# Performance work log

Measured on AMD Instinct MI355X. Metric: run time of the kernel, lower is better.

The kernel has to match this reference:

```python
import jax, jax.numpy as jnp
import numpy as np

EPS = 1e-5
SLOPE = 0.01  # LeakyReLU default negative_slope


def _bn4d(y, g, b):
    # training-mode BatchNorm4d: stats over batch + all 4 spatial dims, biased var
    ax = (0, 2, 3, 4, 5)
    mu = y.mean(axis=ax, keepdims=True)
    var = ((y - mu) ** 2).mean(axis=ax, keepdims=True)
    sh = (1, -1, 1, 1, 1, 1)
    return (y - mu) / jnp.sqrt(var + EPS) * g.reshape(sh) + b.reshape(sh)


def _lrelu(y):
    return jnp.where(y >= 0, y, SLOPE * y)


def setup_inputs() -> dict:
    key = jax.random.key(0)
    ks = jax.random.split(key, 4)
    x = jax.random.uniform(ks[0], (2, 1, 48, 48, 48, 48), dtype=jnp.float32)
    w1 = jax.random.normal(ks[1], (3, 1), dtype=jnp.float32) * 0.5
    w2 = jax.random.normal(ks[2], (6, 3, 2, 2, 2, 2), dtype=jnp.float32) * 0.15
    wt = jax.random.normal(ks[3], (6, 3, 2, 2, 2, 2), dtype=jnp.float32) * 0.15
    return {
        "x": x,
        "w1": w1, "g1": jnp.ones(3, jnp.float32), "b1": jnp.zeros(3, jnp.float32),
        "w2": w2, "g2": jnp.ones(6, jnp.float32), "b2": jnp.zeros(6, jnp.float32),
        "wt": wt, "g3": jnp.ones(3, jnp.float32), "b3": jnp.zeros(3, jnp.float32),
    }


def reference(x, w1, g1, b1, w2, g2, b2, wt, g3, b3):
    # Conv4d(1->3, k=1, s=1, bias=False): pointwise channel mix
    y = jnp.einsum('oc,bcijkl->boijkl', w1, x)
    y = _lrelu(_bn4d(y, g1, b1))

    # Conv4d(3->6, k=2, s=2, bias=False): non-overlapping 2^4 block contraction
    B, C, D1, D2, D3, D4 = y.shape
    yb = y.reshape(B, C, D1 // 2, 2, D2 // 2, 2, D3 // 2, 2, D4 // 2, 2)
    y = jnp.einsum('bcipjqkrls,ocpqrs->boijkl', yb, w2)
    y = _lrelu(_bn4d(y, g2, b2))

    # ConvTranspose4d(6->3, k=2, s=2, bias=False): exact inverse block expansion
    # torch transpose-conv weight layout: (in_ch=6, out_ch=3, 2,2,2,2)
    z = jnp.einsum('bcijkl,copqrs->boipjqkrls', y, wt)
    B, O = z.shape[0], z.shape[1]
    d1, d2, d3, d4 = z.shape[2], z.shape[4], z.shape[6], z.shape[8]
    y = z.reshape(B, O, 2 * d1, 2 * d2, 2 * d3, 2 * d4)
    y = _bn4d(y, g3, b3)
    return jax.nn.sigmoid(y)
```

## Files before the change

kernel.cpp:

```cpp
#include <hip/hip_runtime.h>

#define BATCH 2
#define P1 5308416
#define NX 10616832
#define P2 331776
#define NPOS 663552
#define N2CH 663552.0
#define NZCH 10616832.0
#define EPS 1e-5
#define SLOPE 0.01f
#define NBANK 16

typedef float f32x2 __attribute__((ext_vector_type(2)));


__device__ __forceinline__ float lrelu(float v) { return v >= 0.f ? v : SLOPE * v; }

__device__ __forceinline__ double wred(double v) {
#pragma unroll
    for (int off = 32; off > 0; off >>= 1) v += __shfl_down(v, off, 64);
    return v;
}

__global__ __launch_bounds__(256) void k1_stats_x(const float4* __restrict__ x4,
                                                  double* __restrict__ dx) {
    int gid = blockIdx.x * 256 + threadIdx.x;
    double s = 0.0, q = 0.0;
#pragma unroll 1
    for (int i = gid; i < NX / 4; i += 1296 * 256) {
        float4 v = x4[i];
        s += (double)v.x + (double)v.y + (double)v.z + (double)v.w;
        q += (double)v.x * v.x + (double)v.y * v.y + (double)v.z * v.z + (double)v.w * v.w;
    }
    s = wred(s); q = wred(q);
    __shared__ double lds[4][2];
    int lane = threadIdx.x & 63, wv = threadIdx.x >> 6;
    if (lane == 0) { lds[wv][0] = s; lds[wv][1] = q; }
    __syncthreads();
    if (threadIdx.x < 2) {
        double t = lds[0][threadIdx.x] + lds[1][threadIdx.x] + lds[2][threadIdx.x] + lds[3][threadIdx.x];
        atomicAdd(&dx[(blockIdx.x & (NBANK - 1)) * 2 + threadIdx.x], t);
    }
}

__global__ __launch_bounds__(256) void k2_conv(const float* __restrict__ x,
                                               const float* __restrict__ w1,
                                               const float* __restrict__ g1,
                                               const float* __restrict__ b1,
                                               const float* __restrict__ w2,
                                               const double* __restrict__ dx,
                                               float* __restrict__ y2,
                                               double* __restrict__ d2) {
    double sx = 0.0, qx = 0.0;
#pragma unroll
    for (int bk = 0; bk < NBANK; ++bk) { sx += dx[bk * 2]; qx += dx[bk * 2 + 1]; }
    double mux = sx / (double)NX;
    double vax = qx / (double)NX - mux * mux;
    float a1[3], c1[3];
#pragma unroll
    for (int c = 0; c < 3; ++c) {
        double w = (double)w1[c];
        double inv = 1.0 / sqrt(w * w * vax + EPS);
        double a = w * (double)g1[c] * inv;
        a1[c] = (float)a;
        c1[c] = (float)((double)b1[c] - mux * a);
    }

    double dsum[6] = {0, 0, 0, 0, 0, 0}, dsq[6] = {0, 0, 0, 0, 0, 0};
#pragma unroll 1
    for (int it = 0; it < 4; ++it) {
        int t = blockIdx.x * 256 + threadIdx.x + it * 165888;
        int b = t / P2, rem = t % P2;
        int l0 = rem % 24, t1 = rem / 24;
        int k0 = t1 % 24, t2 = t1 / 24;
        int j0 = t2 % 24, i0 = t2 / 24;
        const float* xb = x + (size_t)b * P1 + (size_t)i0 * 221184 + j0 * 4608 + k0 * 96 + l0 * 2;
        float acc[6] = {0, 0, 0, 0, 0, 0};
#pragma unroll
        for (int p = 0; p < 2; ++p)
#pragma unroll
            for (int q = 0; q < 2; ++q)
#pragma unroll
                for (int r = 0; r < 2; ++r) {
                    const f32x2 xv = *(const f32x2*)(xb + p * 110592 + q * 2304 + r * 48);
#pragma unroll
                    for (int s = 0; s < 2; ++s) {
                        float xs = xv[s];
                        int m = p * 8 + q * 4 + r * 2 + s;
#pragma unroll
                        for (int c = 0; c < 3; ++c) {
                            float tt = lrelu(a1[c] * xs + c1[c]);
#pragma unroll
                            for (int o = 0; o < 6; ++o) acc[o] += w2[o * 48 + c * 16 + m] * tt;
                        }
                    }
                }
#pragma unroll
        for (int o = 0; o < 6; ++o) {
            y2[(size_t)(b * 6 + o) * P2 + rem] = acc[o];
            dsum[o] += (double)acc[o];
            dsq[o] += (double)acc[o] * acc[o];
        }
    }
    __shared__ double lds[4][12];
    int lane = threadIdx.x & 63, wv = threadIdx.x >> 6;
#pragma unroll
    for (int o = 0; o < 6; ++o) {
        double v = wred(dsum[o]); if (lane == 0) lds[wv][o] = v;
        v = wred(dsq[o]);         if (lane == 0) lds[wv][6 + o] = v;
    }
    __syncthreads();
    if (threadIdx.x < 12) {
        double t = lds[0][threadIdx.x] + lds[1][threadIdx.x] + lds[2][threadIdx.x] + lds[3][threadIdx.x];
        atomicAdd(&d2[(blockIdx.x & (NBANK - 1)) * 12 + threadIdx.x], t);
    }
}

__global__ __launch_bounds__(256) void k3_gram(const float* __restrict__ y2,
                                               const float* __restrict__ g2,
                                               const float* __restrict__ b2,
                                               const double* __restrict__ d2,
                                               double* __restrict__ d3) {
    float a2[6], c2[6];
#pragma unroll
    for (int c = 0; c < 6; ++c) {
        double s = 0.0, q = 0.0;
#pragma unroll
        for (int bk = 0; bk < NBANK; ++bk) { s += d2[bk * 12 + c]; q += d2[bk * 12 + 6 + c]; }
        double mu = s / N2CH;
        double va = q / N2CH - mu * mu;
        double a = (double)g2[c] / sqrt(va + EPS);
        a2[c] = (float)a;
        c2[c] = (float)((double)b2[c] - mu * a);
    }
    double S[6] = {0, 0, 0, 0, 0, 0};
    double G[21] = {0};
#pragma unroll 1
    for (int it = 0; it < 4; ++it) {
        int t = blockIdx.x * 256 + threadIdx.x + it * 165888;
        int b = t / P2, rem = t % P2;
        float yn[6];
#pragma unroll
        for (int c = 0; c < 6; ++c) {
            float v = y2[(size_t)(b * 6 + c) * P2 + rem];
            yn[c] = lrelu(a2[c] * v + c2[c]);
            S[c] += (double)yn[c];
        }
        int gi = 0;
#pragma unroll
        for (int c = 0; c < 6; ++c)
#pragma unroll
            for (int cc = c; cc < 6; ++cc) { G[gi] += (double)yn[c] * yn[cc]; ++gi; }
    }
    __shared__ double lds[4][27];
    int lane = threadIdx.x & 63, wv = threadIdx.x >> 6;
#pragma unroll
    for (int i = 0; i < 6; ++i) { double v = wred(S[i]); if (lane == 0) lds[wv][i] = v; }
#pragma unroll
    for (int i = 0; i < 21; ++i) { double v = wred(G[i]); if (lane == 0) lds[wv][6 + i] = v; }
    __syncthreads();
    if (threadIdx.x < 27) {
        double t = lds[0][threadIdx.x] + lds[1][threadIdx.x] + lds[2][threadIdx.x] + lds[3][threadIdx.x];
        atomicAdd(&d3[(blockIdx.x & (NBANK - 1)) * 27 + threadIdx.x], t);
    }
}

__global__ void k4_params(const double* __restrict__ d2, const double* __restrict__ d3,
                          const float* __restrict__ wt,
                          const float* __restrict__ g2v, const float* __restrict__ b2v,
                          const float* __restrict__ g3, const float* __restrict__ b3,
                          float* __restrict__ params) {
    __shared__ double S[6], G[21], s2[12];
    int t = threadIdx.x;
    if (t < 27) {
        double a = 0.0;
        for (int bk = 0; bk < NBANK; ++bk) a += d3[bk * 27 + t];
        if (t < 6) S[t] = a; else G[t - 6] = a;
    }
    if (t >= 32 && t < 44) {
        double a = 0.0;
        for (int bk = 0; bk < NBANK; ++bk) a += d2[bk * 12 + (t - 32)];
        s2[t - 32] = a;
    }
    __syncthreads();
    if (t < 6) {
        int c = t;
        double mu = s2[c] / N2CH;
        double va = s2[6 + c] / N2CH - mu * mu;
        double a = (double)g2v[c] / sqrt(va + EPS);
        params[c] = (float)a;
        params[6 + c] = (float)((double)b2v[c] - mu * a);
    }
    if (t < 3) {
        int o = t;
        double sumz = 0.0, ssq = 0.0;
        for (int c = 0; c < 6; ++c) {
            double wsum = 0.0;
            for (int m = 0; m < 16; ++m) wsum += (double)wt[c * 48 + o * 16 + m];
            sumz += S[c] * wsum;
        }
        for (int c = 0; c < 6; ++c)
            for (int cc = 0; cc < 6; ++cc) {
                double ww = 0.0;
                for (int m = 0; m < 16; ++m) ww += (double)wt[c * 48 + o * 16 + m] * wt[cc * 48 + o * 16 + m];
                int aa = c < cc ? c : cc, bb = c < cc ? cc : c;
                int gidx = aa * 6 - aa * (aa + 1) / 2 + bb;
                ssq += G[gidx] * ww;
            }
        double mu = sumz / NZCH;
        double va = ssq / NZCH - mu * mu;
        double a = (double)g3[o] / sqrt(va + EPS);
        params[12 + o] = (float)a;
        params[15 + o] = (float)((double)b3[o] - mu * a);
    }
}

__global__ __launch_bounds__(256) void k5_expand(const float* __restrict__ y2,
                                                 const float* __restrict__ wt,
                                                 const float* __restrict__ params,
                                                 float* __restrict__ out) {
    int t = blockIdx.x * 256 + threadIdx.x;
    int b = t / P2, rem = t % P2;
    int l0 = rem % 24, t1 = rem / 24;
    int k0 = t1 % 24, t2 = t1 / 24;
    int j0 = t2 % 24, i0 = t2 / 24;
    float yn[6];
#pragma unroll
    for (int c = 0; c < 6; ++c) {
        float v = y2[(size_t)(b * 6 + c) * P2 + rem];
        yn[c] = lrelu(params[c] * v + params[6 + c]);
    }
    size_t obase = (size_t)b * 15925248 + (size_t)i0 * 221184 + j0 * 4608 + k0 * 96 + l0 * 2;
#pragma unroll
    for (int o = 0; o < 3; ++o) {
        float a3 = params[12 + o], c3 = params[15 + o];
#pragma unroll
        for (int p = 0; p < 2; ++p)
#pragma unroll
            for (int q = 0; q < 2; ++q)
#pragma unroll
                for (int r = 0; r < 2; ++r) {
                    f32x2 res;
#pragma unroll
                    for (int s = 0; s < 2; ++s) {
                        int m = p * 8 + q * 4 + r * 2 + s;
                        float z = 0.f;
#pragma unroll
                        for (int c = 0; c < 6; ++c) z += yn[c] * wt[c * 48 + o * 16 + m];
                        float v = a3 * z + c3;
                        res[s] = 1.f / (1.f + __expf(-v));
                    }
                    __builtin_nontemporal_store(res, (f32x2*)(out + obase + (size_t)o * P1 + p * 110592 + q * 2304 + r * 48));
                }
    }
}

extern "C" void kernel_launch(void* const* d_in, const int* in_sizes, int n_in,
                              void* d_out, int out_size, void* d_ws, size_t ws_size,
                              hipStream_t stream) {
    const float* x  = (const float*)d_in[0];
    const float* w1 = (const float*)d_in[1];
    const float* g1 = (const float*)d_in[2];
    const float* b1 = (const float*)d_in[3];
    const float* w2 = (const float*)d_in[4];
    const float* g2 = (const float*)d_in[5];
    const float* b2 = (const float*)d_in[6];
    const float* wt = (const float*)d_in[7];
    const float* g3 = (const float*)d_in[8];
    const float* b3 = (const float*)d_in[9];
    float* out = (float*)d_out;

    char* ws = (char*)d_ws;
    double* dx     = (double*)(ws);
    double* d2     = (double*)(ws + 256);
    double* d3     = (double*)(ws + 1792);
    float*  params = (float*)(ws + 5248);
    float*  y2     = (float*)(ws + 8192);

    (void)hipMemsetAsync(d_ws, 0, 5248, stream);
    k1_stats_x<<<1296, 256, 0, stream>>>((const float4*)x, dx);
    k2_conv<<<648, 256, 0, stream>>>(x, w1, g1, b1, w2, dx, y2, d2);
    k3_gram<<<648, 256, 0, stream>>>(y2, g2, b2, d2, d3);
    k4_params<<<1, 64, 0, stream>>>(d2, d3, wt, g2, b2, g3, b3, params);
    k5_expand<<<2592, 256, 0, stream>>>(y2, wt, params, out);
}
```

Baseline: 362.7 us.

## Vectorize loads/stores, switch per-thread stats to fp32, remap expand threads for contiguous writes

Several kernels are reworked at once. k1 uses a fixed 8-load unrolled loop with fp32 accumulation. k2 has each thread handle two adjacent positions with 16-byte x loads and transposed w2 in LDS, and k3 likewise handles two positions per thread, both with fp32 partial sums. k5 is remapped so each thread writes one 16-byte contiguous output chunk per channel with per-thread weights. The aim is fewer, wider memory transactions and cheaper reductions than double-precision math, at the risk of reduced accuracy in the fp32 partial sums.

```diff
diff --git a/kernel.cpp b/kernel.cpp
--- a/kernel.cpp
+++ b/kernel.cpp
@@ -1,10 +1,8 @@
 #include <hip/hip_runtime.h>
 
-#define BATCH 2
 #define P1 5308416
 #define NX 10616832
 #define P2 331776
-#define NPOS 663552
 #define N2CH 663552.0
 #define NZCH 10616832.0
 #define EPS 1e-5
@@ -12,156 +10,184 @@
 #define NBANK 16
 
 typedef float f32x2 __attribute__((ext_vector_type(2)));
+typedef float f32x4 __attribute__((ext_vector_type(4)));
 
 
 __device__ __forceinline__ float lrelu(float v) { return v >= 0.f ? v : SLOPE * v; }
 
-__device__ __forceinline__ double wred(double v) {
+__device__ __forceinline__ float wredf(float v) {
 #pragma unroll
     for (int off = 32; off > 0; off >>= 1) v += __shfl_down(v, off, 64);
     return v;
 }
 
-__global__ __launch_bounds__(256) void k1_stats_x(const float4* __restrict__ x4,
+__global__ __launch_bounds__(256) void k1_stats_x(const f32x4* __restrict__ x4,
                                                   double* __restrict__ dx) {
     int gid = blockIdx.x * 256 + threadIdx.x;
-    double s = 0.0, q = 0.0;
-#pragma unroll 1
-    for (int i = gid; i < NX / 4; i += 1296 * 256) {
-        float4 v = x4[i];
-        s += (double)v.x + (double)v.y + (double)v.z + (double)v.w;
-        q += (double)v.x * v.x + (double)v.y * v.y + (double)v.z * v.z + (double)v.w * v.w;
-    }
-    s = wred(s); q = wred(q);
-    __shared__ double lds[4][2];
+    float s = 0.f, q = 0.f;
+#pragma unroll
+    for (int k = 0; k < 8; ++k) {
+        f32x4 v = x4[gid + k * 331776];
+        s += v.x + v.y + v.z + v.w;
+        q += v.x * v.x + v.y * v.y + v.z * v.z + v.w * v.w;
+    }
+    s = wredf(s); q = wredf(q);
+    __shared__ float lds[4][2];
     int lane = threadIdx.x & 63, wv = threadIdx.x >> 6;
     if (lane == 0) { lds[wv][0] = s; lds[wv][1] = q; }
     __syncthreads();
     if (threadIdx.x < 2) {
-        double t = lds[0][threadIdx.x] + lds[1][threadIdx.x] + lds[2][threadIdx.x] + lds[3][threadIdx.x];
+        double t = (double)lds[0][threadIdx.x] + lds[1][threadIdx.x] + lds[2][threadIdx.x] + lds[3][threadIdx.x];
         atomicAdd(&dx[(blockIdx.x & (NBANK - 1)) * 2 + threadIdx.x], t);
     }
 }
 
-__global__ __launch_bounds__(256) void k2_conv(const float* __restrict__ x,
-                                               const float* __restrict__ w1,
-                                               const float* __restrict__ g1,
-                                               const float* __restrict__ b1,
-                                               const float* __restrict__ w2,
-                                               const double* __restrict__ dx,
-                                               float* __restrict__ y2,
-                                               double* __restrict__ d2) {
-    double sx = 0.0, qx = 0.0;
-#pragma unroll
-    for (int bk = 0; bk < NBANK; ++bk) { sx += dx[bk * 2]; qx += dx[bk * 2 + 1]; }
-    double mux = sx / (double)NX;
-    double vax = qx / (double)NX - mux * mux;
+__global__ __launch_bounds__(256, 4) void k2_conv(const float* __restrict__ x,
+                                                  const float* __restrict__ w1,
+                                                  const float* __restrict__ g1,
+                                                  const float* __restrict__ b1,
+                                                  const float* __restrict__ w2,
+                                                  const double* __restrict__ dx,
+                                                  float* __restrict__ y2,
+                                                  double* __restrict__ d2) {
+    __shared__ __align__(16) float w2s[48 * 8];
+    __shared__ float p1s[6];
+    for (int idx = threadIdx.x; idx < 288; idx += 256) {
+        int o = idx / 48, cm = idx % 48;
+        w2s[cm * 8 + o] = w2[idx];
+    }
+    if (threadIdx.x < 3) {
+        double sx = 0.0, qx = 0.0;
+#pragma unroll
+        for (int bk = 0; bk < NBANK; ++bk) { sx += dx[bk * 2]; qx += dx[bk * 2 + 1]; }
+        double mux = sx / (double)NX;
+        double vax = qx / (double)NX - mux * mux;
+        int c = threadIdx.x;
+        double w = (double)w1[c];
+        double a = w * (double)g1[c] / sqrt(w * w * vax + EPS);
+        p1s[c] = (float)a;
+        p1s[3 + c] = (float)((double)b1[c] - mux * a);
+    }
+    __syncthreads();
     float a1[3], c1[3];
 #pragma unroll
-    for (int c = 0; c < 3; ++c) {
-        double w = (double)w1[c];
-        double inv = 1.0 / sqrt(w * w * vax + EPS);
-        double a = w * (double)g1[c] * inv;
-        a1[c] = (float)a;
-        c1[c] = (float)((double)b1[c] - mux * a);
-    }
-
-    double dsum[6] = {0, 0, 0, 0, 0, 0}, dsq[6] = {0, 0, 0, 0, 0, 0};
-#pragma unroll 1
-    for (int it = 0; it < 4; ++it) {
-        int t = blockIdx.x * 256 + threadIdx.x + it * 165888;
-        int b = t / P2, rem = t % P2;
-        int l0 = rem % 24, t1 = rem / 24;
-        int k0 = t1 % 24, t2 = t1 / 24;
-        int j0 = t2 % 24, i0 = t2 / 24;
-        const float* xb = x + (size_t)b * P1 + (size_t)i0 * 221184 + j0 * 4608 + k0 * 96 + l0 * 2;
-        float acc[6] = {0, 0, 0, 0, 0, 0};
-#pragma unroll
-        for (int p = 0; p < 2; ++p)
-#pragma unroll
-            for (int q = 0; q < 2; ++q)
-#pragma unroll
-                for (int r = 0; r < 2; ++r) {
-                    const f32x2 xv = *(const f32x2*)(xb + p * 110592 + q * 2304 + r * 48);
-#pragma unroll
-                    for (int s = 0; s < 2; ++s) {
-                        float xs = xv[s];
-                        int m = p * 8 + q * 4 + r * 2 + s;
-#pragma unroll
-                        for (int c = 0; c < 3; ++c) {
-                            float tt = lrelu(a1[c] * xs + c1[c]);
-#pragma unroll
-                            for (int o = 0; o < 6; ++o) acc[o] += w2[o * 48 + c * 16 + m] * tt;
-                        }
-                    }
-                }
-#pragma unroll
-        for (int o = 0; o < 6; ++o) {
-            y2[(size_t)(b * 6 + o) * P2 + rem] = acc[o];
-            dsum[o] += (double)acc[o];
-            dsq[o] += (double)acc[o] * acc[o];
+    for (int c = 0; c < 3; ++c) { a1[c] = p1s[c]; c1[c] = p1s[3 + c]; }
+
+    int t = blockIdx.x * 256 + threadIdx.x;
+    int pos0 = t * 2;
+    int b = pos0 / P2, rem = pos0 % P2;
+    int l0 = rem % 24, t1 = rem / 24;
+    int k0 = t1 % 24, t2 = t1 / 24;
+    int j0 = t2 % 24, i0 = t2 / 24;
+    const float* xb = x + (size_t)b * P1 + (size_t)i0 * 221184 + j0 * 4608 + k0 * 96 + l0 * 2;
+
+    f32x4 xq[8];
+#pragma unroll
+    for (int p = 0; p < 2; ++p)
+#pragma unroll
+        for (int q = 0; q < 2; ++q)
+#pragma unroll
+            for (int r = 0; r < 2; ++r)
+                xq[p * 4 + q * 2 + r] = *(const f32x4*)(xb + p * 110592 + q * 2304 + r * 48);
+
+    float acc0[6] = {0, 0, 0, 0, 0, 0}, acc1[6] = {0, 0, 0, 0, 0, 0};
+#pragma unroll
+    for (int pqr = 0; pqr < 8; ++pqr) {
+#pragma unroll
+        for (int s = 0; s < 2; ++s) {
+            int m = pqr * 2 + s;
+            float xs0 = xq[pqr][s];
+            float xs1 = xq[pqr][2 + s];
+#pragma unroll
+            for (int c = 0; c < 3; ++c) {
+                float tt0 = lrelu(a1[c] * xs0 + c1[c]);
+                float tt1 = lrelu(a1[c] * xs1 + c1[c]);
+                int base = (c * 16 + m) * 8;
+                f32x4 w4 = *(const f32x4*)&w2s[base];
+                f32x2 w2v = *(const f32x2*)&w2s[base + 4];
+                acc0[0] += w4.x * tt0; acc1[0] += w4.x * tt1;
+                acc0[1] += w4.y * tt0; acc1[1] += w4.y * tt1;
+                acc0[2] += w4.z * tt0; acc1[2] += w4.z * tt1;
+                acc0[3] += w4.w * tt0; acc1[3] += w4.w * tt1;
+                acc0[4] += w2v.x * tt0; acc1[4] += w2v.x * tt1;
+                acc0[5] += w2v.y * tt0; acc1[5] += w2v.y * tt1;
+            }
         }
     }
-    __shared__ double lds[4][12];
+    float sum[6], sq[6];
+#pragma unroll
+    for (int o = 0; o < 6; ++o) {
+        f32x2 st; st.x = acc0[o]; st.y = acc1[o];
+        *(f32x2*)(y2 + (size_t)(b * 6 + o) * P2 + rem) = st;
+        sum[o] = acc0[o] + acc1[o];
+        sq[o] = acc0[o] * acc0[o] + acc1[o] * acc1[o];
+    }
+    __shared__ float lds[4][12];
     int lane = threadIdx.x & 63, wv = threadIdx.x >> 6;
 #pragma unroll
     for (int o = 0; o < 6; ++o) {
-        double v = wred(dsum[o]); if (lane == 0) lds[wv][o] = v;
-        v = wred(dsq[o]);         if (lane == 0) lds[wv][6 + o] = v;
+        float v = wredf(sum[o]); if (lane == 0) lds[wv][o] = v;
+        v = wredf(sq[o]);        if (lane == 0) lds[wv][6 + o] = v;
     }
     __syncthreads();
     if (threadIdx.x < 12) {
-        double t = lds[0][threadIdx.x] + lds[1][threadIdx.x] + lds[2][threadIdx.x] + lds[3][threadIdx.x];
-        atomicAdd(&d2[(blockIdx.x & (NBANK - 1)) * 12 + threadIdx.x], t);
-    }
-}
-
-__global__ __launch_bounds__(256) void k3_gram(const float* __restrict__ y2,
-                                               const float* __restrict__ g2,
-                                               const float* __restrict__ b2,
-                                               const double* __restrict__ d2,
-                                               double* __restrict__ d3) {
-    float a2[6], c2[6];
-#pragma unroll
-    for (int c = 0; c < 6; ++c) {
+        double t2d = (double)lds[0][threadIdx.x] + lds[1][threadIdx.x] + lds[2][threadIdx.x] + lds[3][threadIdx.x];
+        atomicAdd(&d2[(blockIdx.x & (NBANK - 1)) * 12 + threadIdx.x], t2d);
+    }
+}
+
+__global__ __launch_bounds__(256, 4) void k3_gram(const float* __restrict__ y2,
+                                                  const float* __restrict__ g2,
+                                                  const float* __restrict__ b2,
+                                                  const double* __restrict__ d2,
+                                                  double* __restrict__ d3) {
+    __shared__ float p2s[12];
+    if (threadIdx.x < 6) {
+        int c = threadIdx.x;
         double s = 0.0, q = 0.0;
 #pragma unroll
         for (int bk = 0; bk < NBANK; ++bk) { s += d2[bk * 12 + c]; q += d2[bk * 12 + 6 + c]; }
         double mu = s / N2CH;
         double va = q / N2CH - mu * mu;
         double a = (double)g2[c] / sqrt(va + EPS);
-        a2[c] = (float)a;
-        c2[c] = (float)((double)b2[c] - mu * a);
-    }
-    double S[6] = {0, 0, 0, 0, 0, 0};
-    double G[21] = {0};
-#pragma unroll 1
-    for (int it = 0; it < 4; ++it) {
-        int t = blockIdx.x * 256 + threadIdx.x + it * 165888;
-        int b = t / P2, rem = t % P2;
-        float yn[6];
-#pragma unroll
-        for (int c = 0; c < 6; ++c) {
-            float v = y2[(size_t)(b * 6 + c) * P2 + rem];
-            yn[c] = lrelu(a2[c] * v + c2[c]);
-            S[c] += (double)yn[c];
-        }
+        p2s[c] = (float)a;
+        p2s[6 + c] = (float)((double)b2[c] - mu * a);
+    }
+    __syncthreads();
+    float a2[6], c2[6];
+#pragma unroll
+    for (int c = 0; c < 6; ++c) { a2[c] = p2s[c]; c2[c] = p2s[6 + c]; }
+
+    int t = blockIdx.x * 256 + threadIdx.x;
+    int pos0 = t * 2;
+    int b = pos0 / P2, rem = pos0 % P2;
+    float yn0[6], yn1[6];
+#pragma unroll
+    for (int c = 0; c < 6; ++c) {
+        f32x2 v = *(const f32x2*)(y2 + (size_t)(b * 6 + c) * P2 + rem);
+        yn0[c] = lrelu(a2[c] * v.x + c2[c]);
+        yn1[c] = lrelu(a2[c] * v.y + c2[c]);
+    }
+    float S[6], G[21];
+#pragma unroll
+    for (int c = 0; c < 6; ++c) S[c] = yn0[c] + yn1[c];
+    {
         int gi = 0;
 #pragma unroll
         for (int c = 0; c < 6; ++c)
 #pragma unroll
-            for (int cc = c; cc < 6; ++cc) { G[gi] += (double)yn[c] * yn[cc]; ++gi; }
-    }
-    __shared__ double lds[4][27];
+            for (int cc = c; cc < 6; ++cc) { G[gi] = yn0[c] * yn0[cc] + yn1[c] * yn1[cc]; ++gi; }
+    }
+    __shared__ float lds[4][27];
     int lane = threadIdx.x & 63, wv = threadIdx.x >> 6;
 #pragma unroll
-    for (int i = 0; i < 6; ++i) { double v = wred(S[i]); if (lane == 0) lds[wv][i] = v; }
-#pragma unroll
-    for (int i = 0; i < 21; ++i) { double v = wred(G[i]); if (lane == 0) lds[wv][6 + i] = v; }
+    for (int i = 0; i < 6; ++i) { float v = wredf(S[i]); if (lane == 0) lds[wv][i] = v; }
+#pragma unroll
+    for (int i = 0; i < 21; ++i) { float v = wredf(G[i]); if (lane == 0) lds[wv][6 + i] = v; }
     __syncthreads();
     if (threadIdx.x < 27) {
-        double t = lds[0][threadIdx.x] + lds[1][threadIdx.x] + lds[2][threadIdx.x] + lds[3][threadIdx.x];
-        atomicAdd(&d3[(blockIdx.x & (NBANK - 1)) * 27 + threadIdx.x], t);
+        double td = (double)lds[0][threadIdx.x] + lds[1][threadIdx.x] + lds[2][threadIdx.x] + lds[3][threadIdx.x];
+        atomicAdd(&d3[(blockIdx.x & (NBANK - 1)) * 27 + threadIdx.x], td);
     }
 }
 
@@ -220,38 +246,58 @@
                                                  const float* __restrict__ params,
                                                  float* __restrict__ out) {
     int t = blockIdx.x * 256 + threadIdx.x;
-    int b = t / P2, rem = t % P2;
-    int l0 = rem % 24, t1 = rem / 24;
-    int k0 = t1 % 24, t2 = t1 / 24;
-    int j0 = t2 % 24, i0 = t2 / 24;
-    float yn[6];
+    int row = t / 12, d = t % 12;
+    int b = row / 110592, rr = row % 110592;
+    int i = rr / 2304, r2 = rr % 2304;
+    int j = r2 / 48, k = r2 % 48;
+    int i0 = i >> 1, p = i & 1;
+    int j0 = j >> 1, q = j & 1;
+    int k0 = k >> 1, r = k & 1;
+
+    float a2[6], c2[6], a3[3], c3[3];
+#pragma unroll
+    for (int c = 0; c < 6; ++c) { a2[c] = params[c]; c2[c] = params[6 + c]; }
+#pragma unroll
+    for (int o = 0; o < 3; ++o) { a3[o] = params[12 + o]; c3[o] = params[15 + o]; }
+
+    float W[3][2][6];
+    int wbase = p * 8 + q * 4 + r * 2;
+#pragma unroll
+    for (int o = 0; o < 3; ++o)
+#pragma unroll
+        for (int s = 0; s < 2; ++s)
+#pragma unroll
+            for (int c = 0; c < 6; ++c)
+                W[o][s][c] = wt[c * 48 + o * 16 + wbase + s];
+
+    const float* yb = y2 + (size_t)b * 6 * P2 + (size_t)i0 * 13824 + j0 * 576 + k0 * 24 + 2 * d;
+    float yn0[6], yn1[6];
 #pragma unroll
     for (int c = 0; c < 6; ++c) {
-        float v = y2[(size_t)(b * 6 + c) * P2 + rem];
-        yn[c] = lrelu(params[c] * v + params[6 + c]);
-    }
-    size_t obase = (size_t)b * 15925248 + (size_t)i0 * 221184 + j0 * 4608 + k0 * 96 + l0 * 2;
+        f32x2 v = *(const f32x2*)(yb + (size_t)c * P2);
+        yn0[c] = lrelu(a2[c] * v.x + c2[c]);
+        yn1[c] = lrelu(a2[c] * v.y + c2[c]);
+    }
+
+    size_t ob = (size_t)b * 15925248 + (size_t)i * 110592 + (size_t)j * 2304 + k * 48 + 4 * d;
 #pragma unroll
     for (int o = 0; o < 3; ++o) {
-        float a3 = params[12 + o], c3 = params[15 + o];
-#pragma unroll
-        for (int p = 0; p < 2; ++p)
-#pragma unroll
-            for (int q = 0; q < 2; ++q)
-#pragma unroll
-                for (int r = 0; r < 2; ++r) {
-                    f32x2 res;
-#pragma unroll
-                    for (int s = 0; s < 2; ++s) {
-                        int m = p * 8 + q * 4 + r * 2 + s;
-                        float z = 0.f;
-#pragma unroll
-                        for (int c = 0; c < 6; ++c) z += yn[c] * wt[c * 48 + o * 16 + m];
-                        float v = a3 * z + c3;
-                        res[s] = 1.f / (1.f + __expf(-v));
-                    }
-                    __builtin_nontemporal_store(res, (f32x2*)(out + obase + (size_t)o * P1 + p * 110592 + q * 2304 + r * 48));
-                }
+        f32x4 res;
+#pragma unroll
+        for (int dd = 0; dd < 4; ++dd) {
+            int s = dd & 1;
+            float z = 0.f;
+            if (dd < 2) {
+#pragma unroll
+                for (int c = 0; c < 6; ++c) z += yn0[c] * W[o][s][c];
+            } else {
+#pragma unroll
+                for (int c = 0; c < 6; ++c) z += yn1[c] * W[o][s][c];
+            }
+            float v = a3[o] * z + c3[o];
+            res[dd] = 1.f / (1.f + __expf(-v));
+        }
+        __builtin_nontemporal_store(res, (f32x4*)(out + ob + (size_t)o * P1));
     }
 }
 
@@ -278,9 +324,9 @@
     float*  y2     = (float*)(ws + 8192);
 
     (void)hipMemsetAsync(d_ws, 0, 5248, stream);
-    k1_stats_x<<<1296, 256, 0, stream>>>((const float4*)x, dx);
-    k2_conv<<<648, 256, 0, stream>>>(x, w1, g1, b1, w2, dx, y2, d2);
-    k3_gram<<<648, 256, 0, stream>>>(y2, g2, b2, d2, d3);
+    k1_stats_x<<<1296, 256, 0, stream>>>((const f32x4*)x, dx);
+    k2_conv<<<1296, 256, 0, stream>>>(x, w1, g1, b1, w2, dx, y2, d2);
+    k3_gram<<<1296, 256, 0, stream>>>(y2, g2, b2, d2, d3);
     k4_params<<<1, 64, 0, stream>>>(d2, d3, wt, g2, b2, g3, b3, params);
-    k5_expand<<<2592, 256, 0, stream>>>(y2, wt, params, out);
-}
+    k5_expand<<<10368, 256, 0, stream>>>(y2, wt, params, out);
+}
```

After: 290.4 us. 1.25x faster.
